# Performance work log

Hardware: AMD Instinct MI355X
Metric: run time of the kernel (lower is better)

## Reference

```python
import jax, jax.numpy as jnp
import numpy as np

B, M, A, C = 32, 32, 3, 80
GRIDS = (13, 26, 52)
IOU_THR = 0.7
L_OBJ, L_NOOBJ, L_COORD = 1.0, 1.0, 0.75
EPS = 1e-8


def _cxcywh_to_xyxy(b):
    cx, cy, w, h = b[..., 0], b[..., 1], b[..., 2], b[..., 3]
    return jnp.stack([cx - w / 2, cy - h / 2, cx + w / 2, cy + h / 2], axis=-1)


def _box_iou(a, b):
    # a: (B,M,4), b: (B,N,4) in xyxy -> (B,M,N)
    lt = jnp.maximum(a[:, :, None, :2], b[:, None, :, :2])
    rb = jnp.minimum(a[:, :, None, 2:], b[:, None, :, 2:])
    wh = jnp.clip(rb - lt, 0.0)
    inter = wh[..., 0] * wh[..., 1]
    area_a = (a[..., 2] - a[..., 0]) * (a[..., 3] - a[..., 1])
    area_b = (b[..., 2] - b[..., 0]) * (b[..., 3] - b[..., 1])
    return inter / (area_a[:, :, None] + area_b[:, None, :] - inter + EPS)


def setup_inputs():
    key = jax.random.key(0)
    ks = jax.random.split(key, 6)
    p0 = jax.random.normal(ks[0], (B, A * (5 + C), GRIDS[0], GRIDS[0]), jnp.float32) * 0.1
    p1 = jax.random.normal(ks[1], (B, A * (5 + C), GRIDS[1], GRIDS[1]), jnp.float32) * 0.1
    p2 = jax.random.normal(ks[2], (B, A * (5 + C), GRIDS[2], GRIDS[2]), jnp.float32) * 0.1
    cxcy = jax.random.uniform(ks[3], (B, M, 2), jnp.float32, 0.05, 0.95)
    wh = jax.random.uniform(ks[4], (B, M, 2), jnp.float32, 0.05, 0.5)
    gt_boxes = jnp.concatenate([cxcy, wh], axis=-1)
    gt_classes = jax.random.randint(ks[5], (B, M), 0, C)
    anchors = jnp.array([[10, 13], [16, 30], [33, 23], [30, 61], [62, 45],
                         [59, 119], [116, 90], [156, 198], [373, 326]], jnp.float32) / 416.0
    return {"p0": p0, "p1": p1, "p2": p2, "gt_boxes": gt_boxes,
            "gt_classes": gt_classes, "anchors": anchors}


def reference(p0, p1, p2, gt_boxes, gt_classes, anchors):
    preds = (p0, p1, p2)
    # ---- global anchor assignment (wh IoU argmax), matches match_anchor ----
    gt_wh = gt_boxes[..., 2:4]                                   # (B,M,2)
    inter = jnp.minimum(gt_wh[:, :, None, :], anchors[None, None]).prod(-1)
    union = gt_wh.prod(-1)[:, :, None] + anchors.prod(-1)[None, None] - inter
    best_prior = jnp.argmax(inter / (union + EPS), axis=-1)      # (B,M) in [0,9)

    cx, cy = gt_boxes[..., 0], gt_boxes[..., 1]
    gt_xyxy = _cxcywh_to_xyxy(gt_boxes)                          # (B,M,4)
    weight = 2.0 - gt_wh.prod(-1)                                # (B,M)

    pred_rows, pos_list, idx_list, t4_list, valid_list = [], [], [], [], []
    nb_off = 0
    for s, G in enumerate(GRIDS):
        ao = s * A
        anch_s = anchors[ao:ao + A]                              # (A,2)
        p = preds[s].reshape(B, A, 5 + C, G, G)
        txy = jax.nn.sigmoid(p[:, :, :2])                        # (B,A,2,G,G)
        twh = p[:, :, 2:4]
        pcls = jax.nn.sigmoid(p[:, :, 4:])
        feat = jnp.concatenate([txy, twh, pcls], axis=2)
        feat = feat.transpose(0, 1, 3, 4, 2).reshape(-1, 5 + C)  # (B*A*G*G, 5+C)
        # ---- decode boxes for matching (no-grad path in original) ----
        xi = jnp.arange(G)[None, None, None, :]                  # along W
        yi = jnp.arange(G)[None, None, :, None]                  # along H
        bcx = (txy[:, :, 0] + xi) / G
        bcy = (txy[:, :, 1] + yi) / G
        bwh = anch_s[None, :, :, None, None] * jnp.exp(twh)      # (B,A,2,G,G)
        boxes = jnp.stack([bcx, bcy, bwh[:, :, 0], bwh[:, :, 1]], axis=-1)
        NBOX = A * G * G
        boxes = _cxcywh_to_xyxy(boxes.reshape(B, NBOX, 4))       # order (A,H,W)
        iou = _box_iou(gt_xyxy, boxes)                           # (B,M,NBOX)
        positivity = jnp.where(iou.max(axis=1) > IOU_THR, 2.0, 0.0)  # (B,NBOX)
        # ---- best-anchor scatter (positivity = 1 overrides) ----
        gx = jnp.clip(jnp.floor(cx * G), 0, G - 1)
        gy = jnp.clip(jnp.floor(cy * G), 0, G - 1)
        dx, dy = cx * G - gx, cy * G - gy                        # cell-fraction offsets
        mask_s = (best_prior >= ao) & (best_prior < ao + A)
        box_idx = ((best_prior - ao) * G * G + gy.astype(jnp.int32) * G
                   + gx.astype(jnp.int32))                       # (B,M)
        flat_box = jnp.arange(B)[:, None] * NBOX + box_idx
        scat_idx = jnp.where(mask_s, flat_box, B * NBOX)         # dummy slot if unmatched
        pos = jnp.concatenate([positivity.reshape(-1), jnp.zeros((1,), positivity.dtype)])
        pos = pos.at[scat_idx.reshape(-1)].set(1.0)[:B * NBOX]
        # ---- encode targets ----
        t_wh = jnp.log(jnp.clip(gt_wh, EPS)) - jnp.log(anchors[best_prior])
        t4 = jnp.concatenate([jnp.stack([dx, dy], -1), t_wh], axis=-1)  # (B,M,4)
        gidx = nb_off + flat_box                                 # global flat pred index
        valid = mask_s & (gidx != 0)                             # mirrors target[:,6].ne(0)
        pred_rows.append(feat)
        pos_list.append(pos)
        idx_list.append(gidx.reshape(-1))
        t4_list.append(t4.reshape(-1, 4))
        valid_list.append(valid.reshape(-1))
        nb_off += B * NBOX

    pred_all = jnp.concatenate(pred_rows)                        # (T, 5+C)
    positivity_all = jax.lax.stop_gradient(jnp.concatenate(pos_list))
    gidx = jnp.concatenate(idx_list)
    t4 = jax.lax.stop_gradient(jnp.concatenate(t4_list))
    valid = jnp.concatenate(valid_list)
    w = jax.lax.stop_gradient(jnp.tile(weight.reshape(-1), 3))
    cls = jnp.tile(gt_classes.reshape(-1), 3)
    v = valid.astype(pred_all.dtype)

    noobj = jnp.sum(jnp.where(positivity_all == 0.0, pred_all[:, 4] ** 2, 0.0))
    pr = pred_all[gidx]                                          # gather positive rows
    coord = jnp.sum(v * w * jnp.sum((pr[:, :4] - t4) ** 2, axis=1))
    obj = jnp.sum(v * (pr[:, 4] - 1.0) ** 2)
    onehot = jax.nn.one_hot(cls, C, dtype=pr.dtype)
    cls_loss = jnp.sum(v[:, None] * (pr[:, 5:] - onehot) ** 2)
    return cls_loss + L_NOOBJ * noobj + L_OBJ * obj + L_COORD * coord
```

## Files before the change

### kernel.cpp

```cpp
#include <hip/hip_runtime.h>
#include <math.h>
#include <float.h>

#define NB 32
#define NM 32
#define NA 3
#define NCLS 80
#define NCH 85
#define IOU_THR 0.7f
#define L_COORD 0.75f
#define FEPS 1e-8f

#define N0_BLKS (NB * NA * 1)
#define N1_BLKS (NB * NA * 1)
#define N2_BLKS (NB * NA * 3)
#define OFF1 (N0_BLKS)
#define OFF2 (OFF1 + N1_BLKS)
#define OFFM (OFF2 + N2_BLKS)
#define MATCHED_TASKS (3 * NB * NM / 4)
#define TOTAL_TASKS (OFFM + MATCHED_TASKS)

struct Smem {
    float4 sbox[NM];
    float  sarea[NM];
    int    scode[NM];
    int    slist[NM];
    int    clist[NM];
    float  wmin[4], wmax[4];
    int    scnt, ccnt;
    float  wsum[4];
};

__device__ __forceinline__ float sigmoidf_(float x) {
    return 1.0f / (1.0f + expf(-x));
}

__device__ __forceinline__ int best_prior(const float* __restrict__ anchors,
                                          float w, float h, float area_g) {
    float best = -1.0f;
    int bp = 0;
    #pragma unroll
    for (int k = 0; k < 9; ++k) {
        float aw = anchors[k * 2 + 0];
        float ah = anchors[k * 2 + 1];
        float inter = fminf(w, aw) * fminf(h, ah);
        float uni = area_g + aw * ah - inter;
        float r = inter / (uni + FEPS);
        if (r > best) { best = r; bp = k; }
    }
    return bp;
}

template <int G, int S, int CHUNKS_, int VEC>
__device__ float noobj_body(const float* __restrict__ p,
                            const float* __restrict__ gt_boxes,
                            const float* __restrict__ anchors,
                            int bid, Smem& sm) {
    constexpr int GG = G * G;
    constexpr int CHUNK = 256 * VEC;
    static_assert(VEC == 1 || (GG % 4 == 0), "float4 path needs GG%4==0");

    int chunk = bid % CHUNKS_;
    int a = (bid / CHUNKS_) % NA;
    int b = bid / (CHUNKS_ * NA);
    int tid = threadIdx.x;
    int lane = tid & 63, wid = tid >> 6;

    if (tid < NM) {
        int e = b * NM + tid;
        float cx = gt_boxes[e * 4 + 0];
        float cy = gt_boxes[e * 4 + 1];
        float w  = gt_boxes[e * 4 + 2];
        float h  = gt_boxes[e * 4 + 3];
        float x1 = cx - w * 0.5f, y1 = cy - h * 0.5f;
        float x2 = cx + w * 0.5f, y2 = cy + h * 0.5f;
        sm.sbox[tid] = make_float4(x1, y1, x2, y2);
        sm.sarea[tid] = (x2 - x1) * (y2 - y1);
        int bp = best_prior(anchors, w, h, w * h);
        int code = -1;
        if (bp >= S * NA && bp < S * NA + NA) {
            float gxf = fminf(fmaxf(floorf(cx * (float)G), 0.0f), (float)(G - 1));
            float gyf = fminf(fmaxf(floorf(cy * (float)G), 0.0f), (float)(G - 1));
            code = (bp - S * NA) * GG + (int)gyf * G + (int)gxf;
        }
        sm.scode[tid] = code;
    }

    float aw = anchors[(S * NA + a) * 2 + 0];
    float ah = anchors[(S * NA + a) * 2 + 1];
    int cell0 = chunk * CHUNK + tid * VEC;
    bool live = cell0 < GG;
    const float* cb = p + (size_t)(b * (NA * NCH) + a * NCH) * GG + cell0;

    float twv[VEC], thv[VEC], tov[VEC], bw[VEC], bh[VEC], areab[VEC];
    float mn = FLT_MAX, mx = 0.0f;
    if (live) {
        if constexpr (VEC == 4) {
            float4 t2 = *reinterpret_cast<const float4*>(cb + 2 * (size_t)GG);
            float4 t3 = *reinterpret_cast<const float4*>(cb + 3 * (size_t)GG);
            float4 t4 = *reinterpret_cast<const float4*>(cb + 4 * (size_t)GG);
            twv[0]=t2.x; twv[1]=t2.y; twv[2]=t2.z; twv[3]=t2.w;
            thv[0]=t3.x; thv[1]=t3.y; thv[2]=t3.z; thv[3]=t3.w;
            tov[0]=t4.x; tov[1]=t4.y; tov[2]=t4.z; tov[3]=t4.w;
        } else {
            twv[0] = cb[2 * (size_t)GG];
            thv[0] = cb[3 * (size_t)GG];
            tov[0] = cb[4 * (size_t)GG];
        }
        #pragma unroll
        for (int v = 0; v < VEC; ++v) {
            bw[v] = aw * expf(twv[v]);
            bh[v] = ah * expf(thv[v]);
            areab[v] = bw[v] * bh[v];
            mn = fminf(mn, areab[v]);
            mx = fmaxf(mx, areab[v]);
        }
    }

    #pragma unroll
    for (int off = 32; off; off >>= 1) {
        mn = fminf(mn, __shfl_xor(mn, off));
        mx = fmaxf(mx, __shfl_xor(mx, off));
    }
    if (lane == 0) { sm.wmin[wid] = mn; sm.wmax[wid] = mx; }
    __syncthreads();

    if (tid < 64) {
        float bmin = fminf(fminf(sm.wmin[0], sm.wmin[1]), fminf(sm.wmin[2], sm.wmin[3]));
        float bmax = fmaxf(fmaxf(sm.wmax[0], sm.wmax[1]), fmaxf(sm.wmax[2], sm.wmax[3]));
        bool c_win = false, c_code = false;
        int cellcode = 0;
        if (tid < NM) {
            float Am = sm.sarea[tid];
            c_win = (1.02f * bmax > IOU_THR * Am) && (1.02f * Am > IOU_THR * bmin);
            int code = sm.scode[tid];
            c_code = (code >= a * GG) && (code < (a + 1) * GG);
            cellcode = code - a * GG;
        }
        unsigned long long mwin = __ballot(c_win);
        unsigned long long mcode = __ballot(c_code);
        unsigned long long below = (1ull << tid) - 1;
        if (c_win)  sm.slist[__popcll(mwin & below)] = tid;
        if (c_code) sm.clist[__popcll(mcode & below)] = cellcode;
        if (tid == 0) { sm.scnt = (int)__popcll(mwin); sm.ccnt = (int)__popcll(mcode); }
    }
    __syncthreads();

    int sc = sm.scnt, cc = sm.ccnt;
    int posm = 0;

    for (int j = 0; j < cc; ++j) {
        int code = sm.clist[j];
        #pragma unroll
        for (int v = 0; v < VEC; ++v) posm |= (code == cell0 + v) ? (1 << v) : 0;
    }

    if (sc > 0 && live) {
        float tx[VEC], ty[VEC];
        if constexpr (VEC == 4) {
            float4 t0 = *reinterpret_cast<const float4*>(cb);
            float4 t1 = *reinterpret_cast<const float4*>(cb + (size_t)GG);
            tx[0]=t0.x; tx[1]=t0.y; tx[2]=t0.z; tx[3]=t0.w;
            ty[0]=t1.x; ty[1]=t1.y; ty[2]=t1.z; ty[3]=t1.w;
        } else {
            tx[0] = cb[0];
            ty[0] = cb[(size_t)GG];
        }
        float bx1[VEC], by1[VEC], bx2[VEC], by2[VEC];
        #pragma unroll
        for (int v = 0; v < VEC; ++v) {
            int cell = cell0 + v;
            int gy = cell / G, gx = cell - gy * G;
            float bcx = (sigmoidf_(tx[v]) + (float)gx) / (float)G;
            float bcy = (sigmoidf_(ty[v]) + (float)gy) / (float)G;
            bx1[v] = bcx - bw[v] * 0.5f; by1[v] = bcy - bh[v] * 0.5f;
            bx2[v] = bcx + bw[v] * 0.5f; by2[v] = bcy + bh[v] * 0.5f;
        }
        for (int j = 0; j < sc; ++j) {
            int m = sm.slist[j];
            float4 bb = sm.sbox[m];
            float am = sm.sarea[m];
            #pragma unroll
            for (int v = 0; v < VEC; ++v) {
                float ltx = fmaxf(bb.x, bx1[v]), lty = fmaxf(bb.y, by1[v]);
                float rbx = fminf(bb.z, bx2[v]), rby = fminf(bb.w, by2[v]);
                float wx = fmaxf(rbx - ltx, 0.0f), wy = fmaxf(rby - lty, 0.0f);
                float inter = wx * wy;
                float denom = am + areab[v] - inter + FEPS;
                posm |= (inter > IOU_THR * denom) ? (1 << v) : 0;
            }
        }
    }

    float local = 0.0f;
    if (live) {
        #pragma unroll
        for (int v = 0; v < VEC; ++v) {
            if (!((posm >> v) & 1)) {
                float so = sigmoidf_(tov[v]);
                local += so * so;
            }
        }
    }

    for (int off = 32; off; off >>= 1) local += __shfl_down(local, off);
    if (lane == 0) sm.wsum[wid] = local;
    __syncthreads();
    return sm.wsum[0] + sm.wsum[1] + sm.wsum[2] + sm.wsum[3];
}

__device__ float matched_body(const float* __restrict__ p0,
                              const float* __restrict__ p1,
                              const float* __restrict__ p2,
                              const float* __restrict__ gt_boxes,
                              const int* __restrict__ gt_classes,
                              const float* __restrict__ anchors,
                              int mb, Smem& sm) {
    int tid = threadIdx.x;
    int wave = tid >> 6, lane = tid & 63;
    int t = mb * 4 + wave;
    int s = t >> 10;
    int e = t & 1023;
    int b = e >> 5;

    float cx = gt_boxes[e * 4 + 0];
    float cy = gt_boxes[e * 4 + 1];
    float w  = gt_boxes[e * 4 + 2];
    float h  = gt_boxes[e * 4 + 3];
    int bp = best_prior(anchors, w, h, w * h);
    int a = bp - s * NA;

    float term = 0.0f;
    if (a >= 0 && a < NA) {
        const float* p = (s == 0) ? p0 : ((s == 1) ? p1 : p2);
        int G = (s == 0) ? 13 : ((s == 1) ? 26 : 52);
        long nboff = (s == 0) ? 0L : ((s == 1) ? 16224L : 81120L);
        int GG = G * G;

        float gxf = fminf(fmaxf(floorf(cx * (float)G), 0.0f), (float)(G - 1));
        float gyf = fminf(fmaxf(floorf(cy * (float)G), 0.0f), (float)(G - 1));
        int gx = (int)gxf, gy = (int)gyf;
        int box_idx = a * GG + gy * G + gx;
        long gidx = nboff + (long)b * (NA * GG) + box_idx;
        if (gidx != 0) {
            float dx = cx * (float)G - gxf;
            float dy = cy * (float)G - gyf;
            float wgt = 2.0f - w * h;
            float twt = logf(fmaxf(w, FEPS)) - logf(anchors[bp * 2 + 0]);
            float tht = logf(fmaxf(h, FEPS)) - logf(anchors[bp * 2 + 1]);
            int cls = gt_classes[e];

            size_t cellbase = (size_t)(b * (NA * NCH) + a * NCH) * GG
                              + (size_t)(gy * G + gx);
            for (int ch = lane; ch < NCH; ch += 64) {
                float val = p[cellbase + (size_t)ch * GG];
                if (ch < 2) {
                    float sv = sigmoidf_(val);
                    float d = sv - (ch == 0 ? dx : dy);
                    term += L_COORD * wgt * d * d;
                } else if (ch < 4) {
                    float d = val - (ch == 2 ? twt : tht);
                    term += L_COORD * wgt * d * d;
                } else if (ch == 4) {
                    float sv = sigmoidf_(val);
                    term += (sv - 1.0f) * (sv - 1.0f);
                } else {
                    float sv = sigmoidf_(val);
                    float oh = ((ch - 5) == cls) ? 1.0f : 0.0f;
                    term += (sv - oh) * (sv - oh);
                }
            }
        }
    }

    for (int off = 32; off; off >>= 1) term += __shfl_down(term, off);
    if (lane == 0) sm.wsum[wave] = term;
    __syncthreads();
    return sm.wsum[0] + sm.wsum[1] + sm.wsum[2] + sm.wsum[3];
}

__device__ __forceinline__ float do_task(int task,
        const float* __restrict__ p0, const float* __restrict__ p1,
        const float* __restrict__ p2, const float* __restrict__ gt_boxes,
        const int* __restrict__ gt_classes, const float* __restrict__ anchors,
        Smem& sm) {
    if (task < OFF1)      return noobj_body<13, 0, 1, 1>(p0, gt_boxes, anchors, task, sm);
    else if (task < OFF2) return noobj_body<26, 1, 1, 4>(p1, gt_boxes, anchors, task - OFF1, sm);
    else if (task < OFFM) return noobj_body<52, 2, 3, 4>(p2, gt_boxes, anchors, task - OFF2, sm);
    else return matched_body(p0, p1, p2, gt_boxes, gt_classes, anchors, task - OFFM, sm);
}

__global__ __launch_bounds__(256)
void yolo_fused(const float* __restrict__ p0, const float* __restrict__ p1,
                const float* __restrict__ p2, const float* __restrict__ gt_boxes,
                const int* __restrict__ gt_classes, const float* __restrict__ anchors,
                float* __restrict__ partials) {
    __shared__ Smem sm;
    float part = do_task(blockIdx.x, p0, p1, p2, gt_boxes, gt_classes, anchors, sm);
    if (threadIdx.x == 0) partials[blockIdx.x] = part;
}

__global__ __launch_bounds__(256)
void yolo_reduce(const float* __restrict__ partials, float* __restrict__ out) {
    int tid = threadIdx.x;
    float s = 0.0f;
    for (int i = tid; i < TOTAL_TASKS; i += 256) s += partials[i];
    for (int off = 32; off; off >>= 1) s += __shfl_down(s, off);
    __shared__ float wsum[4];
    if ((tid & 63) == 0) wsum[tid >> 6] = s;
    __syncthreads();
    if (tid == 0) out[0] = wsum[0] + wsum[1] + wsum[2] + wsum[3];
}

extern "C" void kernel_launch(void* const* d_in, const int* in_sizes, int n_in,
                              void* d_out, int out_size, void* d_ws, size_t ws_size,
                              hipStream_t stream) {
    const float* p0 = (const float*)d_in[0];
    const float* p1 = (const float*)d_in[1];
    const float* p2 = (const float*)d_in[2];
    const float* gt_boxes = (const float*)d_in[3];
    const int* gt_classes = (const int*)d_in[4];
    const float* anchors = (const float*)d_in[5];
    float* out = (float*)d_out;
    float* partials = (float*)d_ws;

    yolo_fused<<<TOTAL_TASKS, 256, 0, stream>>>(p0, p1, p2, gt_boxes,
                                                gt_classes, anchors, partials);
    yolo_reduce<<<1, 256, 0, stream>>>(partials, out);
}
```

Measured before the change: 19.55 us.

## Assign one matched task per GT and hoist all prediction loads early

The matched-loss phase previously launched one wave per (scale, GT) pair, and two thirds of those waves found no matching anchor and idled. Each wave now handles one GT and derives the scale from its best prior, which cuts the matched blocks to a third of the previous count. Separately, the noobj body now issues all five channel loads (tx, ty, tw, th, obj) before the GT/shared-memory setup so their latency overlaps it. The cost is more live registers, and tx/ty are now loaded even when no IoU test is needed.

```diff
diff --git a/kernel.cpp b/kernel.cpp
--- a/kernel.cpp
+++ b/kernel.cpp
@@ -17,8 +17,8 @@
 #define OFF1 (N0_BLKS)
 #define OFF2 (OFF1 + N1_BLKS)
 #define OFFM (OFF2 + N2_BLKS)
-#define MATCHED_TASKS (3 * NB * NM / 4)
-#define TOTAL_TASKS (OFFM + MATCHED_TASKS)
+#define MATCHED_BLKS (NB * NM / 4)
+#define TOTAL_TASKS (OFFM + MATCHED_BLKS)
 
 struct Smem {
     float4 sbox[NM];
@@ -65,6 +65,34 @@
     int b = bid / (CHUNKS_ * NA);
     int tid = threadIdx.x;
     int lane = tid & 63, wid = tid >> 6;
+
+    float aw = anchors[(S * NA + a) * 2 + 0];
+    float ah = anchors[(S * NA + a) * 2 + 1];
+    int cell0 = chunk * CHUNK + tid * VEC;
+    bool live = cell0 < GG;
+    const float* cb = p + (size_t)(b * (NA * NCH) + a * NCH) * GG + cell0;
+
+    float txv[VEC], tyv[VEC], twv[VEC], thv[VEC], tov[VEC];
+    if (live) {
+        if constexpr (VEC == 4) {
+            float4 t0 = *reinterpret_cast<const float4*>(cb);
+            float4 t1 = *reinterpret_cast<const float4*>(cb + (size_t)GG);
+            float4 t2 = *reinterpret_cast<const float4*>(cb + 2 * (size_t)GG);
+            float4 t3 = *reinterpret_cast<const float4*>(cb + 3 * (size_t)GG);
+            float4 t4 = *reinterpret_cast<const float4*>(cb + 4 * (size_t)GG);
+            txv[0]=t0.x; txv[1]=t0.y; txv[2]=t0.z; txv[3]=t0.w;
+            tyv[0]=t1.x; tyv[1]=t1.y; tyv[2]=t1.z; tyv[3]=t1.w;
+            twv[0]=t2.x; twv[1]=t2.y; twv[2]=t2.z; twv[3]=t2.w;
+            thv[0]=t3.x; thv[1]=t3.y; thv[2]=t3.z; thv[3]=t3.w;
+            tov[0]=t4.x; tov[1]=t4.y; tov[2]=t4.z; tov[3]=t4.w;
+        } else {
+            txv[0] = cb[0];
+            tyv[0] = cb[(size_t)GG];
+            twv[0] = cb[2 * (size_t)GG];
+            thv[0] = cb[3 * (size_t)GG];
+            tov[0] = cb[4 * (size_t)GG];
+        }
+    }
 
     if (tid < NM) {
         int e = b * NM + tid;
@@ -86,27 +114,9 @@
         sm.scode[tid] = code;
     }
 
-    float aw = anchors[(S * NA + a) * 2 + 0];
-    float ah = anchors[(S * NA + a) * 2 + 1];
-    int cell0 = chunk * CHUNK + tid * VEC;
-    bool live = cell0 < GG;
-    const float* cb = p + (size_t)(b * (NA * NCH) + a * NCH) * GG + cell0;
-
-    float twv[VEC], thv[VEC], tov[VEC], bw[VEC], bh[VEC], areab[VEC];
+    float bw[VEC], bh[VEC], areab[VEC];
     float mn = FLT_MAX, mx = 0.0f;
     if (live) {
-        if constexpr (VEC == 4) {
-            float4 t2 = *reinterpret_cast<const float4*>(cb + 2 * (size_t)GG);
-            float4 t3 = *reinterpret_cast<const float4*>(cb + 3 * (size_t)GG);
-            float4 t4 = *reinterpret_cast<const float4*>(cb + 4 * (size_t)GG);
-            twv[0]=t2.x; twv[1]=t2.y; twv[2]=t2.z; twv[3]=t2.w;
-            thv[0]=t3.x; thv[1]=t3.y; thv[2]=t3.z; thv[3]=t3.w;
-            tov[0]=t4.x; tov[1]=t4.y; tov[2]=t4.z; tov[3]=t4.w;
-        } else {
-            twv[0] = cb[2 * (size_t)GG];
-            thv[0] = cb[3 * (size_t)GG];
-            tov[0] = cb[4 * (size_t)GG];
-        }
         #pragma unroll
         for (int v = 0; v < VEC; ++v) {
             bw[v] = aw * expf(twv[v]);
@@ -116,7 +126,6 @@
             mx = fmaxf(mx, areab[v]);
         }
     }
-
     #pragma unroll
     for (int off = 32; off; off >>= 1) {
         mn = fminf(mn, __shfl_xor(mn, off));
@@ -156,23 +165,13 @@
     }
 
     if (sc > 0 && live) {
-        float tx[VEC], ty[VEC];
-        if constexpr (VEC == 4) {
-            float4 t0 = *reinterpret_cast<const float4*>(cb);
-            float4 t1 = *reinterpret_cast<const float4*>(cb + (size_t)GG);
-            tx[0]=t0.x; tx[1]=t0.y; tx[2]=t0.z; tx[3]=t0.w;
-            ty[0]=t1.x; ty[1]=t1.y; ty[2]=t1.z; ty[3]=t1.w;
-        } else {
-            tx[0] = cb[0];
-            ty[0] = cb[(size_t)GG];
-        }
         float bx1[VEC], by1[VEC], bx2[VEC], by2[VEC];
         #pragma unroll
         for (int v = 0; v < VEC; ++v) {
             int cell = cell0 + v;
             int gy = cell / G, gx = cell - gy * G;
-            float bcx = (sigmoidf_(tx[v]) + (float)gx) / (float)G;
-            float bcy = (sigmoidf_(ty[v]) + (float)gy) / (float)G;
+            float bcx = (sigmoidf_(txv[v]) + (float)gx) / (float)G;
+            float bcy = (sigmoidf_(tyv[v]) + (float)gy) / (float)G;
             bx1[v] = bcx - bw[v] * 0.5f; by1[v] = bcy - bh[v] * 0.5f;
             bx2[v] = bcx + bw[v] * 0.5f; by2[v] = bcy + bh[v] * 0.5f;
         }
@@ -218,9 +217,7 @@
                               int mb, Smem& sm) {
     int tid = threadIdx.x;
     int wave = tid >> 6, lane = tid & 63;
-    int t = mb * 4 + wave;
-    int s = t >> 10;
-    int e = t & 1023;
+    int e = mb * 4 + wave;
     int b = e >> 5;
 
     float cx = gt_boxes[e * 4 + 0];
@@ -228,47 +225,47 @@
     float w  = gt_boxes[e * 4 + 2];
     float h  = gt_boxes[e * 4 + 3];
     int bp = best_prior(anchors, w, h, w * h);
-    int a = bp - s * NA;
+    int s = bp / 3;
+    int a = bp - s * 3;
+
+    const float* p = (s == 0) ? p0 : ((s == 1) ? p1 : p2);
+    int G = (s == 0) ? 13 : ((s == 1) ? 26 : 52);
+    long nboff = (s == 0) ? 0L : ((s == 1) ? 16224L : 81120L);
+    int GG = G * G;
+
+    float gxf = fminf(fmaxf(floorf(cx * (float)G), 0.0f), (float)(G - 1));
+    float gyf = fminf(fmaxf(floorf(cy * (float)G), 0.0f), (float)(G - 1));
+    int gx = (int)gxf, gy = (int)gyf;
+    int box_idx = a * GG + gy * G + gx;
+    long gidx = nboff + (long)b * (NA * GG) + box_idx;
 
     float term = 0.0f;
-    if (a >= 0 && a < NA) {
-        const float* p = (s == 0) ? p0 : ((s == 1) ? p1 : p2);
-        int G = (s == 0) ? 13 : ((s == 1) ? 26 : 52);
-        long nboff = (s == 0) ? 0L : ((s == 1) ? 16224L : 81120L);
-        int GG = G * G;
-
-        float gxf = fminf(fmaxf(floorf(cx * (float)G), 0.0f), (float)(G - 1));
-        float gyf = fminf(fmaxf(floorf(cy * (float)G), 0.0f), (float)(G - 1));
-        int gx = (int)gxf, gy = (int)gyf;
-        int box_idx = a * GG + gy * G + gx;
-        long gidx = nboff + (long)b * (NA * GG) + box_idx;
-        if (gidx != 0) {
-            float dx = cx * (float)G - gxf;
-            float dy = cy * (float)G - gyf;
-            float wgt = 2.0f - w * h;
-            float twt = logf(fmaxf(w, FEPS)) - logf(anchors[bp * 2 + 0]);
-            float tht = logf(fmaxf(h, FEPS)) - logf(anchors[bp * 2 + 1]);
-            int cls = gt_classes[e];
-
-            size_t cellbase = (size_t)(b * (NA * NCH) + a * NCH) * GG
-                              + (size_t)(gy * G + gx);
-            for (int ch = lane; ch < NCH; ch += 64) {
-                float val = p[cellbase + (size_t)ch * GG];
-                if (ch < 2) {
-                    float sv = sigmoidf_(val);
-                    float d = sv - (ch == 0 ? dx : dy);
-                    term += L_COORD * wgt * d * d;
-                } else if (ch < 4) {
-                    float d = val - (ch == 2 ? twt : tht);
-                    term += L_COORD * wgt * d * d;
-                } else if (ch == 4) {
-                    float sv = sigmoidf_(val);
-                    term += (sv - 1.0f) * (sv - 1.0f);
-                } else {
-                    float sv = sigmoidf_(val);
-                    float oh = ((ch - 5) == cls) ? 1.0f : 0.0f;
-                    term += (sv - oh) * (sv - oh);
-                }
+    if (gidx != 0) {
+        float dx = cx * (float)G - gxf;
+        float dy = cy * (float)G - gyf;
+        float wgt = 2.0f - w * h;
+        float twt = logf(fmaxf(w, FEPS)) - logf(anchors[bp * 2 + 0]);
+        float tht = logf(fmaxf(h, FEPS)) - logf(anchors[bp * 2 + 1]);
+        int cls = gt_classes[e];
+
+        size_t cellbase = (size_t)(b * (NA * NCH) + a * NCH) * GG
+                          + (size_t)(gy * G + gx);
+        for (int ch = lane; ch < NCH; ch += 64) {
+            float val = p[cellbase + (size_t)ch * GG];
+            if (ch < 2) {
+                float sv = sigmoidf_(val);
+                float d = sv - (ch == 0 ? dx : dy);
+                term += L_COORD * wgt * d * d;
+            } else if (ch < 4) {
+                float d = val - (ch == 2 ? twt : tht);
+                term += L_COORD * wgt * d * d;
+            } else if (ch == 4) {
+                float sv = sigmoidf_(val);
+                term += (sv - 1.0f) * (sv - 1.0f);
+            } else {
+                float sv = sigmoidf_(val);
+                float oh = ((ch - 5) == cls) ? 1.0f : 0.0f;
+                term += (sv - oh) * (sv - oh);
             }
         }
     }
```

Result: faster. 19.00 us (-2.8%).
